# Kernel tuning notes

Hardware: AMD Instinct MI355X
Metric: run time of the kernel (lower is better)

Reference implementation:

```python
import jax, jax.numpy as jnp
import numpy as np
from jax import lax

EPS = 1e-5
DN = ('NCHW', 'OIHW', 'NCHW')

def _sign(v):
    # (v >= 0) * 2 - 1
    return jnp.where(v >= 0, 1.0, -1.0).astype(v.dtype)

def _conv(x, w, b):
    y = lax.conv_general_dilated(x, w, (1, 1), 'VALID', dimension_numbers=DN)
    return y + b[None, :, None, None]

def _bn(x):
    # BatchNorm2d(affine=False), training mode: biased batch stats over (N,H,W)
    m = jnp.mean(x, axis=(0, 2, 3), keepdims=True)
    v = jnp.var(x, axis=(0, 2, 3), keepdims=True)
    return (x - m) * lax.rsqrt(v + EPS)

def setup_inputs() -> dict:
    key = jax.random.key(0)
    ks = jax.random.split(key, 9)
    f = jnp.float32
    B = 8192
    x = jax.random.normal(ks[0], (B, 1, 28, 28), dtype=f)
    # conv params, clipped to [-1, 1] as in clip_weights()
    w1 = jnp.clip(jax.random.normal(ks[1], (32, 1, 9, 9), dtype=f) * 0.1, -1, 1)
    b1 = jnp.clip(jax.random.normal(ks[2], (32,), dtype=f) * 0.1, -1, 1)
    w2 = jnp.clip(jax.random.normal(ks[3], (16, 32, 9, 9), dtype=f) * 0.1, -1, 1)
    b2 = jnp.clip(jax.random.normal(ks[4], (16,), dtype=f) * 0.1, -1, 1)
    w3 = jnp.clip(jax.random.normal(ks[5], (8, 16, 9, 9), dtype=f) * 0.1, -1, 1)
    b3 = jnp.clip(jax.random.normal(ks[6], (8,), dtype=f) * 0.1, -1, 1)
    wl = jnp.clip(jax.random.normal(ks[7], (10, 8, 4, 4), dtype=f) * 0.1, -1, 1)
    bl = jnp.clip(jax.random.normal(ks[8], (10,), dtype=f) * 0.1, -1, 1)
    return {"x": x, "w1": w1, "b1": b1, "w2": w2, "b2": b2,
            "w3": w3, "b3": b3, "wl": wl, "bl": bl}

def _block(x, w, b, act=True, norm=True, binarized=True):
    if binarized:
        w, b = _sign(w), _sign(b)
    x = _conv(x, w, b)
    if norm:
        x = _bn(x)
    if act:
        x = _sign(x) if binarized else jax.nn.relu(x)
    return x

def reference(x, w1, b1, w2, b2, w3, b3, wl, bl):
    x = _sign(x)                        # binarize input activations
    x = _block(x, w1, b1)               # (B, 32, 20, 20)
    x = _block(x, w2, b2)               # (B, 16, 12, 12)
    x = _block(x, w3, b3)               # (B,  8,  4,  4)
    x = _block(x, wl, bl, act=False, norm=False)  # (B, 10, 1, 1), binarized weights
    return x.reshape(-1, 10)
```

## Files before the change

### kernel.cpp

```cpp
#include <hip/hip_runtime.h>
#include <stdint.h>

#define BATCH 8192

#define OFF_W1R3    0
#define OFF_W2T     1152
#define OFF_W3B     6336
#define OFF_WLB     8928
#define OFF_SBL     9088
#define OFF_TTOT    9216
#define OFF_T2      9600
#define OFF_S3      9664
#define OFF_S2PART  9728
#define OFF_Z2      534528
#define OFF_Z3      38283264

__global__ __launch_bounds__(256) void k0_pack(const float* __restrict__ w1,
                                               const float* __restrict__ w2,
                                               const float* __restrict__ w3,
                                               const float* __restrict__ wl,
                                               const float* __restrict__ bl,
                                               uint8_t* __restrict__ ws) {
  uint32_t* W1R3 = (uint32_t*)(ws + OFF_W1R3);
  uint32_t* W2T  = (uint32_t*)(ws + OFF_W2T);
  uint32_t* W3B  = (uint32_t*)(ws + OFF_W3B);
  uint64_t* WLB  = (uint64_t*)(ws + OFF_WLB);
  float*    SBL  = (float*)(ws + OFF_SBL);
  int tid = threadIdx.x;
  for (int e = tid; e < 96; e += 256) {
    int oc = e / 3, i = e % 3;
    uint32_t m = 0;
    for (int rr = 0; rr < 3; ++rr)
      for (int kw = 0; kw < 9; ++kw)
        if (w1[oc*81 + (3*i+rr)*9 + kw] < 0.f) m |= 1u << (rr*9 + kw);
    W1R3[e] = m;
  }
  for (int e = tid; e < 1296; e += 256) {
    int k = e >> 4, oc = e & 15;
    uint32_t m = 0;
    for (int ic = 0; ic < 32; ++ic)
      if (w2[(oc*32 + ic)*81 + k] < 0.f) m |= 1u << ic;
    W2T[e] = m;
  }
  for (int e = tid; e < 648; e += 256) {
    int oc = e / 81, k = e % 81;
    uint32_t m = 0;
    for (int ic = 0; ic < 16; ++ic)
      if (w3[(oc*16 + ic)*81 + k] < 0.f) m |= 1u << ic;
    W3B[e] = m;
  }
  for (int e = tid; e < 20; e += 256) {
    int oc = e >> 1, word = e & 1;
    uint64_t m = 0;
    for (int b = 0; b < 64; ++b)
      if (wl[oc*128 + word*64 + b] < 0.f) m |= 1ull << b;
    WLB[e] = m;
  }
  if (tid < 10) SBL[tid] = (bl[tid] >= 0.f) ? 1.f : -1.f;
}

__global__ __launch_bounds__(256) void k1_tsum(const float* __restrict__ x,
                                               uint8_t* __restrict__ ws) {
  int* Ttot = (int*)(ws + OFF_TTOT);
  __shared__ uint16_t RP[4][28][29];
  __shared__ uint16_t P[4][29][29];
  __shared__ int Tacc[81];
  const int tid = threadIdx.x;
  const int wv = tid >> 6, ln = tid & 63;
  if (tid < 81) Tacc[tid] = 0;
  __syncthreads();
  for (int it = 0; it < 2; ++it) {
    int img = blockIdx.x * 8 + it * 4 + wv;
    const float* xi = x + (size_t)img * 784;
    if (ln < 28) {
      uint16_t cnt = 0;
      RP[wv][ln][0] = 0;
      for (int c = 0; c < 28; ++c) {
        cnt += (xi[ln*28 + c] < 0.f) ? 1 : 0;
        RP[wv][ln][c+1] = cnt;
      }
    }
    __syncthreads();
    if (ln < 29) {
      uint16_t run = 0;
      P[wv][0][ln] = 0;
      for (int i = 1; i <= 28; ++i) {
        run += RP[wv][i-1][ln];
        P[wv][i][ln] = run;
      }
    }
    __syncthreads();
    if (ln < 81) {
      int kh = ln / 9, kw = ln % 9;
      int cnt = (int)P[wv][kh+20][kw+20] - (int)P[wv][kh][kw+20]
              - (int)P[wv][kh+20][kw]  + (int)P[wv][kh][kw];
      atomicAdd(&Tacc[ln], 400 - 2*cnt);
    }
    __syncthreads();
  }
  if (tid < 81) atomicAdd(&Ttot[tid], Tacc[tid]);
}

#define K2_IMGS 8
__global__ __launch_bounds__(256) void k2_conv12(const float* __restrict__ x,
                                                 uint8_t* __restrict__ ws) {
  const uint32_t* W1R3g = (const uint32_t*)(ws + OFF_W1R3);
  const uint32_t* W2Tg  = (const uint32_t*)(ws + OFF_W2T);
  const int* Ttot = (const int*)(ws + OFF_TTOT);
  int* S2P = (int*)(ws + OFF_S2PART);

  __shared__ uint32_t __attribute__((aligned(16))) rowm[K2_IMGS*28];
  __shared__ uint32_t __attribute__((aligned(16))) w1r3[96];
  __shared__ uint32_t __attribute__((aligned(16))) w2t[1296];
  __shared__ int tlds[81];
  __shared__ int t1s[32];
  __shared__ uint32_t __attribute__((aligned(16))) A1s[K2_IMGS*400];
  __shared__ int s2acc[16];

  const int tid = threadIdx.x;
  const int img0 = blockIdx.x * K2_IMGS;

  for (int e = tid; e < 96; e += 256)   w1r3[e] = W1R3g[e];
  for (int e = tid; e < 1296; e += 256) w2t[e]  = W2Tg[e];
  if (tid < 81) tlds[tid] = Ttot[tid];
  if (tid < 16) s2acc[tid] = 0;
  if (tid < K2_IMGS*28) {
    int il = tid / 28, rr = tid % 28;
    const float4* xr = (const float4*)(x + (size_t)(img0 + il) * 784 + rr * 28);
    uint32_t m = 0;
    #pragma unroll
    for (int j = 0; j < 7; ++j) {
      float4 v = xr[j];
      if (v.x < 0.f) m |= 1u << (j*4+0);
      if (v.y < 0.f) m |= 1u << (j*4+1);
      if (v.z < 0.f) m |= 1u << (j*4+2);
      if (v.w < 0.f) m |= 1u << (j*4+3);
    }
    rowm[tid] = m;
  }
  __syncthreads();

  if (tid < 32) {
    long long S = 0;
    for (int kh = 0; kh < 9; ++kh)
      for (int kw = 0; kw < 9; ++kw) {
        int bit = (w1r3[tid*3 + kh/3] >> ((kh%3)*9 + kw)) & 1;
        S += (long long)(1 - 2*bit) * tlds[kh*9 + kw];
      }
    const long long N1 = (long long)BATCH * 400;
    long long q = S / N1, rr = S % N1;
    long long t = q + (rr > 0 ? 1 : 0);
    if ((t & 1) == 0) t += 1;
    t1s[tid] = (int)t;
  }
  __syncthreads();

  for (int G = tid; G < K2_IMGS*80; G += 256) {
    int il = G / 80, rem = G - il*80;
    int oh = rem >> 2, ow0 = (rem & 3) * 5;
    uint32_t R[9];
    #pragma unroll
    for (int i = 0; i < 9; ++i) R[i] = rowm[il*28 + oh + i];
    uint32_t win[5][3];
    #pragma unroll
    for (int j = 0; j < 5; ++j) {
      int ow = ow0 + j;
      #pragma unroll
      for (int i = 0; i < 3; ++i) {
        uint32_t b0 = (R[3*i]   >> ow) & 0x1FFu;
        uint32_t b1 = (R[3*i+1] >> ow) & 0x1FFu;
        uint32_t b2 = (R[3*i+2] >> ow) & 0x1FFu;
        win[j][i] = b0 | (b1 << 9) | (b2 << 18);
      }
    }
    uint32_t mask[5] = {0,0,0,0,0};
    #pragma unroll
    for (int ocg = 0; ocg < 4; ++ocg) {
      const uint4* wp = (const uint4*)&w1r3[ocg*24];
      uint32_t wr[24];
      #pragma unroll
      for (int q = 0; q < 6; ++q) {
        uint4 v = wp[q];
        wr[q*4+0]=v.x; wr[q*4+1]=v.y; wr[q*4+2]=v.z; wr[q*4+3]=v.w;
      }
      #pragma unroll
      for (int o8 = 0; o8 < 8; ++o8) {
        int oc = ocg*8 + o8;
        int t = t1s[oc];
        #pragma unroll
        for (int j = 0; j < 5; ++j) {
          int mm = __popc(win[j][0] ^ wr[o8*3])
                 + __popc(win[j][1] ^ wr[o8*3+1])
                 + __popc(win[j][2] ^ wr[o8*3+2]);
          mask[j] |= (uint32_t)((81 - 2*mm) < t) << oc;
        }
      }
    }
    #pragma unroll
    for (int j = 0; j < 5; ++j) A1s[il*400 + oh*20 + ow0 + j] = mask[j];
  }
  __syncthreads();

  uint32_t* Z2w = (uint32_t*)(ws + OFF_Z2);
  const int och = tid & 7, oc0 = och << 1;
  int sl0 = 0, sl1 = 0;
  for (int r = 0; r < 3; ++r) {
    int G = tid + r*256;
    int il = G / 96, rem = G - il*96;
    int oy = rem >> 3;
    const uint32_t* A = &A1s[il*400 + oy*20];
    int acc0[12], acc1[12];
    #pragma unroll
    for (int p = 0; p < 12; ++p) { acc0[p] = 0; acc1[p] = 0; }
    for (int kh = 0; kh < 9; ++kh) {
      const uint4* ar = (const uint4*)(A + kh*20);
      uint32_t a[20];
      #pragma unroll
      for (int q = 0; q < 5; ++q) {
        uint4 v = ar[q];
        a[q*4+0]=v.x; a[q*4+1]=v.y; a[q*4+2]=v.z; a[q*4+3]=v.w;
      }
      uint32_t wv0[9], wv1[9];
      #pragma unroll
      for (int kw = 0; kw < 9; ++kw) {
        uint2 wv = *(const uint2*)&w2t[(kh*9 + kw)*16 + oc0];
        wv0[kw] = wv.x; wv1[kw] = wv.y;
      }
      #pragma unroll
      for (int kw = 0; kw < 9; ++kw) {
        #pragma unroll
        for (int px = 0; px < 12; ++px) {
          acc0[px] += __popc(a[kw+px] ^ wv0[kw]);
          acc1[px] += __popc(a[kw+px] ^ wv1[kw]);
        }
      }
    }
    size_t base0 = (size_t)(img0+il)*1152 + (size_t)oc0*72 + oy*6;
    uint32_t u0[6], u1[6];
    #pragma unroll
    for (int h2 = 0; h2 < 6; ++h2) {
      int za = 2592 - 2*acc0[2*h2], zb = 2592 - 2*acc0[2*h2+1];
      sl0 += za + zb;
      u0[h2] = (uint32_t)(uint16_t)(int16_t)za | ((uint32_t)(uint16_t)(int16_t)zb << 16);
      int zc = 2592 - 2*acc1[2*h2], zd = 2592 - 2*acc1[2*h2+1];
      sl1 += zc + zd;
      u1[h2] = (uint32_t)(uint16_t)(int16_t)zc | ((uint32_t)(uint16_t)(int16_t)zd << 16);
    }
    uint2* p0 = (uint2*)(Z2w + base0);
    p0[0] = make_uint2(u0[0], u0[1]); p0[1] = make_uint2(u0[2], u0[3]); p0[2] = make_uint2(u0[4], u0[5]);
    uint2* p1 = (uint2*)(Z2w + base0 + 72);
    p1[0] = make_uint2(u1[0], u1[1]); p1[1] = make_uint2(u1[2], u1[3]); p1[2] = make_uint2(u1[4], u1[5]);
  }
  atomicAdd(&s2acc[oc0],   sl0);
  atomicAdd(&s2acc[oc0+1], sl1);
  __syncthreads();
  if (tid < 16) S2P[blockIdx.x*16 + tid] = s2acc[tid];
}

__global__ __launch_bounds__(256) void k2b_reduce(uint8_t* __restrict__ ws) {
  const int* S2P = (const int*)(ws + OFF_S2PART);
  int* T2 = (int*)(ws + OFF_T2);
  __shared__ long long part[256];
  int tid = threadIdx.x;
  int c = tid & 15, g = tid >> 4;
  long long s = 0;
  for (int b = g*64; b < g*64 + 64; ++b) s += S2P[b*16 + c];
  part[tid] = s;
  __syncthreads();
  if (tid < 16) {
    long long S = 0;
    for (int g2 = 0; g2 < 16; ++g2) S += part[g2*16 + tid];
    const long long N2 = (long long)BATCH * 144;
    long long q = S / N2, r = S % N2;
    long long t = q + (r > 0 ? 1 : 0);
    if (t & 1) t += 1;
    T2[tid] = (int)t;
  }
}

__global__ __launch_bounds__(256) void k3_conv3(uint8_t* __restrict__ ws) {
  const int16_t* Z2 = (const int16_t*)(ws + OFF_Z2);
  const int* T2 = (const int*)(ws + OFF_T2);
  const uint32_t* W3Bg = (const uint32_t*)(ws + OFF_W3B);
  int16_t* Z3 = (int16_t*)(ws + OFF_Z3);
  unsigned long long* S3 = (unsigned long long*)(ws + OFF_S3);

  __shared__ uint32_t w3b[648];
  __shared__ int t2[16];
  __shared__ uint32_t A2[2][144];
  __shared__ int s3acc[8];

  const int tid = threadIdx.x;
  for (int e = tid; e < 648; e += 256) w3b[e] = W3Bg[e];
  if (tid < 16) t2[tid] = T2[tid];
  if (tid < 8) s3acc[tid] = 0;
  __syncthreads();

  const int half = tid >> 7, h = tid & 127;
  for (int it = 0; it < 4; ++it) {
    int img = blockIdx.x * 8 + it*2 + half;
    const int16_t* z2i = Z2 + (size_t)img * 2304;
    for (int p = h; p < 144; p += 128) {
      uint32_t m = 0;
      #pragma unroll
      for (int ic = 0; ic < 16; ++ic)
        if ((int)z2i[ic*144 + p] < t2[ic]) m |= 1u << ic;
      A2[half][p] = m;
    }
    __syncthreads();
    {
      int oc = h >> 4, pix = h & 15;
      int oy = pix >> 2, ox = pix & 3;
      int mism = 0;
      for (int kh = 0; kh < 9; ++kh)
        #pragma unroll
        for (int kw = 0; kw < 9; ++kw)
          mism += __popc(A2[half][(oy+kh)*12 + ox + kw] ^ w3b[oc*81 + kh*9 + kw]);
      int z3 = 1296 - 2*mism;
      Z3[(size_t)img*128 + h] = (int16_t)z3;
      atomicAdd(&s3acc[oc], z3);
    }
    __syncthreads();
  }
  if (tid < 8)
    atomicAdd(&S3[tid], (unsigned long long)(long long)s3acc[tid]);
}

__global__ __launch_bounds__(256) void k4_final(uint8_t* __restrict__ ws,
                                               float* __restrict__ out) {
  const int16_t* Z3 = (const int16_t*)(ws + OFF_Z3);
  const long long* S3 = (const long long*)(ws + OFF_S3);
  const uint64_t* WLBg = (const uint64_t*)(ws + OFF_WLB);
  const float* SBLg = (const float*)(ws + OFF_SBL);
  __shared__ int t3[8];
  __shared__ uint64_t wlb[20];
  __shared__ float sbl[10];
  const int tid = threadIdx.x;
  if (tid < 8) {
    long long S = S3[tid];
    const long long N3 = (long long)BATCH * 16;
    long long q = S / N3, r = S % N3;
    long long t = q + (r > 0 ? 1 : 0);
    if (t & 1) t += 1;
    t3[tid] = (int)t;
  }
  if (tid < 20) wlb[tid] = WLBg[tid];
  if (tid < 10) sbl[tid] = SBLg[tid];
  __syncthreads();
  int img = blockIdx.x * 256 + tid;
  const int16_t* z3i = Z3 + (size_t)img * 128;
  uint64_t a0 = 0, a1 = 0;
  for (int j = 0; j < 64; ++j)
    if ((int)z3i[j] < t3[j >> 4]) a0 |= 1ull << j;
  for (int j = 0; j < 64; ++j)
    if ((int)z3i[64 + j] < t3[(64 + j) >> 4]) a1 |= 1ull << j;
  #pragma unroll
  for (int oc = 0; oc < 10; ++oc) {
    int mism = __popcll(a0 ^ wlb[oc*2]) + __popcll(a1 ^ wlb[oc*2 + 1]);
    out[(size_t)img*10 + oc] = (float)(128 - 2*mism) + sbl[oc];
  }
}

extern "C" void kernel_launch(void* const* d_in, const int* in_sizes, int n_in,
                              void* d_out, int out_size, void* d_ws, size_t ws_size,
                              hipStream_t stream) {
  (void)in_sizes; (void)n_in; (void)out_size; (void)ws_size;
  const float* x  = (const float*)d_in[0];
  const float* w1 = (const float*)d_in[1];
  const float* w2 = (const float*)d_in[3];
  const float* w3 = (const float*)d_in[5];
  const float* wl = (const float*)d_in[7];
  const float* bl = (const float*)d_in[8];
  uint8_t* ws = (uint8_t*)d_ws;
  float* out = (float*)d_out;

  hipMemsetAsync(ws + OFF_TTOT, 0, 512, stream);
  k0_pack<<<1, 256, 0, stream>>>(w1, w2, w3, wl, bl, ws);
  k1_tsum<<<1024, 256, 0, stream>>>(x, ws);
  k2_conv12<<<1024, 256, 0, stream>>>(x, ws);
  k2b_reduce<<<1, 256, 0, stream>>>(ws);
  k3_conv3<<<1024, 256, 0, stream>>>(ws);
  k4_final<<<32, 256, 0, stream>>>(ws, out);
}
```

Before: 301.5 us.

## Fuse pack/reduce kernels, use bitmask popcount tsum, repack Z2/Z3 layouts

Folds weight packing into the input-statistics kernel and recomputes the input window sums from row bitmasks with popcount and a sliding window, instead of 2D prefix sums in shared memory. The separate BN2 reduction kernel is merged into conv3, which now handles 32 images per block. Z2 is switched to a pixel-major interleaved layout so conv3 can build its bitmasks from vectorized loads, and Z3 is read with uint4 loads. These changes cut kernel launches and strided global reads, but every conv3 block now redundantly re-reduces the S2 partial sums, and the padded weight layouts must match their indexing exactly.

After: 257.8 us. 1.17x faster.

```diff
diff --git a/kernel.cpp b/kernel.cpp
--- a/kernel.cpp
+++ b/kernel.cpp
@@ -3,101 +3,125 @@
 
 #define BATCH 8192
 
-#define OFF_W1R3    0
-#define OFF_W2T     1152
-#define OFF_W3B     6336
-#define OFF_WLB     8928
-#define OFF_SBL     9088
-#define OFF_TTOT    9216
-#define OFF_T2      9600
-#define OFF_S3      9664
-#define OFF_S2PART  9728
-#define OFF_Z2      534528
-#define OFF_Z3      38283264
-
-__global__ __launch_bounds__(256) void k0_pack(const float* __restrict__ w1,
-                                               const float* __restrict__ w2,
-                                               const float* __restrict__ w3,
-                                               const float* __restrict__ wl,
-                                               const float* __restrict__ bl,
-                                               uint8_t* __restrict__ ws) {
-  uint32_t* W1R3 = (uint32_t*)(ws + OFF_W1R3);
-  uint32_t* W2T  = (uint32_t*)(ws + OFF_W2T);
-  uint32_t* W3B  = (uint32_t*)(ws + OFF_W3B);
-  uint64_t* WLB  = (uint64_t*)(ws + OFF_WLB);
-  float*    SBL  = (float*)(ws + OFF_SBL);
-  int tid = threadIdx.x;
-  for (int e = tid; e < 96; e += 256) {
-    int oc = e / 3, i = e % 3;
-    uint32_t m = 0;
-    for (int rr = 0; rr < 3; ++rr)
-      for (int kw = 0; kw < 9; ++kw)
-        if (w1[oc*81 + (3*i+rr)*9 + kw] < 0.f) m |= 1u << (rr*9 + kw);
-    W1R3[e] = m;
-  }
-  for (int e = tid; e < 1296; e += 256) {
-    int k = e >> 4, oc = e & 15;
-    uint32_t m = 0;
-    for (int ic = 0; ic < 32; ++ic)
-      if (w2[(oc*32 + ic)*81 + k] < 0.f) m |= 1u << ic;
-    W2T[e] = m;
-  }
-  for (int e = tid; e < 648; e += 256) {
-    int oc = e / 81, k = e % 81;
-    uint32_t m = 0;
-    for (int ic = 0; ic < 16; ++ic)
-      if (w3[(oc*16 + ic)*81 + k] < 0.f) m |= 1u << ic;
-    W3B[e] = m;
-  }
-  for (int e = tid; e < 20; e += 256) {
-    int oc = e >> 1, word = e & 1;
-    uint64_t m = 0;
-    for (int b = 0; b < 64; ++b)
-      if (wl[oc*128 + word*64 + b] < 0.f) m |= 1ull << b;
-    WLB[e] = m;
-  }
-  if (tid < 10) SBL[tid] = (bl[tid] >= 0.f) ? 1.f : -1.f;
-}
-
-__global__ __launch_bounds__(256) void k1_tsum(const float* __restrict__ x,
-                                               uint8_t* __restrict__ ws) {
+#define OFF_W1R3   0
+#define OFF_W2P    384
+#define OFF_W3P    6144
+#define OFF_WLB    9600
+#define OFF_SBL    9760
+#define OFF_TTOT   9856
+#define OFF_S3     10184
+#define OFF_S2PART 10496
+#define OFF_Z2     76800
+#define OFF_Z3     37825792
+
+__global__ __launch_bounds__(256) void k1_pack_tsum(const float* __restrict__ x,
+                                                    const float* __restrict__ w1,
+                                                    const float* __restrict__ w2,
+                                                    const float* __restrict__ w3,
+                                                    const float* __restrict__ wl,
+                                                    const float* __restrict__ bl,
+                                                    uint8_t* __restrict__ ws) {
   int* Ttot = (int*)(ws + OFF_TTOT);
-  __shared__ uint16_t RP[4][28][29];
-  __shared__ uint16_t P[4][29][29];
+  const int tid = threadIdx.x;
+
+  if (blockIdx.x == 0) {
+    uint32_t* W1R3 = (uint32_t*)(ws + OFF_W1R3);
+    uint32_t* W2P  = (uint32_t*)(ws + OFF_W2P);
+    uint32_t* W3P  = (uint32_t*)(ws + OFF_W3P);
+    uint64_t* WLB  = (uint64_t*)(ws + OFF_WLB);
+    float*    SBL  = (float*)(ws + OFF_SBL);
+    for (int e = tid; e < 96; e += 256) {
+      int oc = e / 3, i = e % 3;
+      uint32_t m = 0;
+      for (int rr = 0; rr < 3; ++rr)
+        for (int kw = 0; kw < 9; ++kw)
+          if (w1[oc*81 + (3*i+rr)*9 + kw] < 0.f) m |= 1u << (rr*9 + kw);
+      W1R3[e] = m;
+    }
+    for (int e = tid; e < 648; e += 256) {
+      int och = e / 81, k = e % 81;
+      int kh = k / 9, kw = k % 9;
+      uint32_t m0 = 0, m1 = 0;
+      int oc0 = och*2;
+      for (int ic = 0; ic < 32; ++ic) {
+        if (w2[(oc0*32 + ic)*81 + k] < 0.f)     m0 |= 1u << ic;
+        if (w2[((oc0+1)*32 + ic)*81 + k] < 0.f) m1 |= 1u << ic;
+      }
+      int idx = ((och*9 + kh)*10 + kw)*2;
+      W2P[idx] = m0; W2P[idx+1] = m1;
+    }
+    for (int e = tid; e < 72; e += 256) {
+      int idx = (e*10 + 9)*2;
+      W2P[idx] = 0; W2P[idx+1] = 0;
+    }
+    for (int e = tid; e < 648; e += 256) {
+      int oc = e / 81, k = e % 81;
+      int kh = k / 9, kw = k % 9;
+      uint32_t m = 0;
+      for (int ic = 0; ic < 16; ++ic)
+        if (w3[(oc*16 + ic)*81 + k] < 0.f) m |= 1u << ic;
+      W3P[(oc*9 + kh)*12 + kw] = m;
+    }
+    for (int e = tid; e < 216; e += 256) {
+      int row = e / 3, p = e % 3;
+      W3P[row*12 + 9 + p] = 0;
+    }
+    for (int e = tid; e < 20; e += 256) {
+      int oc = e >> 1, word = e & 1;
+      uint64_t m = 0;
+      for (int b = 0; b < 64; ++b)
+        if (wl[oc*128 + word*64 + b] < 0.f) m |= 1ull << b;
+      WLB[e] = m;
+    }
+    if (tid < 10) SBL[tid] = (bl[tid] >= 0.f) ? 1.f : -1.f;
+  }
+
+  __shared__ uint32_t rowm[896];
   __shared__ int Tacc[81];
-  const int tid = threadIdx.x;
-  const int wv = tid >> 6, ln = tid & 63;
   if (tid < 81) Tacc[tid] = 0;
   __syncthreads();
-  for (int it = 0; it < 2; ++it) {
-    int img = blockIdx.x * 8 + it * 4 + wv;
-    const float* xi = x + (size_t)img * 784;
-    if (ln < 28) {
-      uint16_t cnt = 0;
-      RP[wv][ln][0] = 0;
-      for (int c = 0; c < 28; ++c) {
-        cnt += (xi[ln*28 + c] < 0.f) ? 1 : 0;
-        RP[wv][ln][c+1] = cnt;
-      }
-    }
-    __syncthreads();
-    if (ln < 29) {
-      uint16_t run = 0;
-      P[wv][0][ln] = 0;
-      for (int i = 1; i <= 28; ++i) {
-        run += RP[wv][i-1][ln];
-        P[wv][i][ln] = run;
-      }
-    }
-    __syncthreads();
-    if (ln < 81) {
-      int kh = ln / 9, kw = ln % 9;
-      int cnt = (int)P[wv][kh+20][kw+20] - (int)P[wv][kh][kw+20]
-              - (int)P[wv][kh+20][kw]  + (int)P[wv][kh][kw];
-      atomicAdd(&Tacc[ln], 400 - 2*cnt);
-    }
-    __syncthreads();
-  }
+
+  const int img0 = blockIdx.x * 32;
+  #pragma unroll
+  for (int it = 0; it < 4; ++it) {
+    int R = tid + it*256;
+    if (R < 896) {
+      int il = R / 28, r = R % 28;
+      const float4* xr = (const float4*)(x + (size_t)(img0 + il) * 784 + r * 28);
+      uint32_t m = 0;
+      #pragma unroll
+      for (int j = 0; j < 7; ++j) {
+        float4 v = xr[j];
+        if (v.x < 0.f) m |= 1u << (j*4+0);
+        if (v.y < 0.f) m |= 1u << (j*4+1);
+        if (v.z < 0.f) m |= 1u << (j*4+2);
+        if (v.w < 0.f) m |= 1u << (j*4+3);
+      }
+      rowm[R] = m;
+    }
+  }
+  __syncthreads();
+
+  for (int T = tid; T < 288; T += 256) {
+    int il = T / 9, kw = T % 9;
+    int base = il * 28;
+    int n9[9];
+    int sum20 = 0;
+    #pragma unroll
+    for (int r = 0; r < 20; ++r) {
+      int n = __popc((rowm[base + r] >> kw) & 0xFFFFFu);
+      if (r < 9) n9[r] = n;
+      sum20 += n;
+    }
+    atomicAdd(&Tacc[kw], 400 - 2*sum20);
+    #pragma unroll
+    for (int kh = 1; kh <= 8; ++kh) {
+      int nadd = __popc((rowm[base + kh + 19] >> kw) & 0xFFFFFu);
+      sum20 += nadd - n9[kh-1];
+      atomicAdd(&Tacc[kh*9 + kw], 400 - 2*sum20);
+    }
+  }
+  __syncthreads();
   if (tid < 81) atomicAdd(&Ttot[tid], Tacc[tid]);
 }
 
@@ -105,13 +129,13 @@
 __global__ __launch_bounds__(256) void k2_conv12(const float* __restrict__ x,
                                                  uint8_t* __restrict__ ws) {
   const uint32_t* W1R3g = (const uint32_t*)(ws + OFF_W1R3);
-  const uint32_t* W2Tg  = (const uint32_t*)(ws + OFF_W2T);
+  const uint32_t* W2Pg  = (const uint32_t*)(ws + OFF_W2P);
   const int* Ttot = (const int*)(ws + OFF_TTOT);
   int* S2P = (int*)(ws + OFF_S2PART);
 
   __shared__ uint32_t __attribute__((aligned(16))) rowm[K2_IMGS*28];
   __shared__ uint32_t __attribute__((aligned(16))) w1r3[96];
-  __shared__ uint32_t __attribute__((aligned(16))) w2t[1296];
+  __shared__ uint32_t __attribute__((aligned(16))) w2p[1440];
   __shared__ int tlds[81];
   __shared__ int t1s[32];
   __shared__ uint32_t __attribute__((aligned(16))) A1s[K2_IMGS*400];
@@ -121,7 +145,7 @@
   const int img0 = blockIdx.x * K2_IMGS;
 
   for (int e = tid; e < 96; e += 256)   w1r3[e] = W1R3g[e];
-  for (int e = tid; e < 1296; e += 256) w2t[e]  = W2Tg[e];
+  for (int e = tid; e < 1440; e += 256) w2p[e]  = W2Pg[e];
   if (tid < 81) tlds[tid] = Ttot[tid];
   if (tid < 16) s2acc[tid] = 0;
   if (tid < K2_IMGS*28) {
@@ -220,36 +244,31 @@
         uint4 v = ar[q];
         a[q*4+0]=v.x; a[q*4+1]=v.y; a[q*4+2]=v.z; a[q*4+3]=v.w;
       }
-      uint32_t wv0[9], wv1[9];
+      const uint4* wp4 = (const uint4*)&w2p[(och*9 + kh)*20];
+      uint32_t wbuf[20];
+      #pragma unroll
+      for (int q = 0; q < 5; ++q) {
+        uint4 v = wp4[q];
+        wbuf[q*4+0]=v.x; wbuf[q*4+1]=v.y; wbuf[q*4+2]=v.z; wbuf[q*4+3]=v.w;
+      }
       #pragma unroll
       for (int kw = 0; kw < 9; ++kw) {
-        uint2 wv = *(const uint2*)&w2t[(kh*9 + kw)*16 + oc0];
-        wv0[kw] = wv.x; wv1[kw] = wv.y;
-      }
-      #pragma unroll
-      for (int kw = 0; kw < 9; ++kw) {
+        uint32_t w0 = wbuf[2*kw], w1v = wbuf[2*kw+1];
         #pragma unroll
         for (int px = 0; px < 12; ++px) {
-          acc0[px] += __popc(a[kw+px] ^ wv0[kw]);
-          acc1[px] += __popc(a[kw+px] ^ wv1[kw]);
+          acc0[px] += __popc(a[kw+px] ^ w0);
+          acc1[px] += __popc(a[kw+px] ^ w1v);
         }
       }
     }
-    size_t base0 = (size_t)(img0+il)*1152 + (size_t)oc0*72 + oy*6;
-    uint32_t u0[6], u1[6];
-    #pragma unroll
-    for (int h2 = 0; h2 < 6; ++h2) {
-      int za = 2592 - 2*acc0[2*h2], zb = 2592 - 2*acc0[2*h2+1];
-      sl0 += za + zb;
-      u0[h2] = (uint32_t)(uint16_t)(int16_t)za | ((uint32_t)(uint16_t)(int16_t)zb << 16);
-      int zc = 2592 - 2*acc1[2*h2], zd = 2592 - 2*acc1[2*h2+1];
-      sl1 += zc + zd;
-      u1[h2] = (uint32_t)(uint16_t)(int16_t)zc | ((uint32_t)(uint16_t)(int16_t)zd << 16);
-    }
-    uint2* p0 = (uint2*)(Z2w + base0);
-    p0[0] = make_uint2(u0[0], u0[1]); p0[1] = make_uint2(u0[2], u0[3]); p0[2] = make_uint2(u0[4], u0[5]);
-    uint2* p1 = (uint2*)(Z2w + base0 + 72);
-    p1[0] = make_uint2(u1[0], u1[1]); p1[1] = make_uint2(u1[2], u1[3]); p1[2] = make_uint2(u1[4], u1[5]);
+    size_t wbase = (size_t)(img0+il)*1152 + (size_t)oy*96 + och;
+    #pragma unroll
+    for (int px = 0; px < 12; ++px) {
+      int z0 = 2592 - 2*acc0[px], z1v = 2592 - 2*acc1[px];
+      sl0 += z0; sl1 += z1v;
+      Z2w[wbase + px*8] = (uint32_t)(uint16_t)(int16_t)z0
+                        | ((uint32_t)(uint16_t)(int16_t)z1v << 16);
+    }
   }
   atomicAdd(&s2acc[oc0],   sl0);
   atomicAdd(&s2acc[oc0+1], sl1);
@@ -257,78 +276,107 @@
   if (tid < 16) S2P[blockIdx.x*16 + tid] = s2acc[tid];
 }
 
-__global__ __launch_bounds__(256) void k2b_reduce(uint8_t* __restrict__ ws) {
+__global__ __launch_bounds__(256) void k3_conv3(uint8_t* __restrict__ ws) {
   const int* S2P = (const int*)(ws + OFF_S2PART);
-  int* T2 = (int*)(ws + OFF_T2);
-  __shared__ long long part[256];
-  int tid = threadIdx.x;
-  int c = tid & 15, g = tid >> 4;
-  long long s = 0;
-  for (int b = g*64; b < g*64 + 64; ++b) s += S2P[b*16 + c];
-  part[tid] = s;
+  const uint32_t* W3Pg = (const uint32_t*)(ws + OFF_W3P);
+  const uint32_t* Z2w = (const uint32_t*)(ws + OFF_Z2);
+  uint32_t* Z3w = (uint32_t*)(ws + OFF_Z3);
+  unsigned long long* S3 = (unsigned long long*)(ws + OFF_S3);
+
+  __shared__ uint32_t __attribute__((aligned(16))) w3p[864];
+  __shared__ int part[256];
+  __shared__ int t2s[16];
+  __shared__ uint32_t __attribute__((aligned(16))) A2[32*144];
+  __shared__ int s3acc[8];
+
+  const int tid = threadIdx.x;
+  const int img0 = blockIdx.x * 32;
+
+  {
+    int c = tid & 15, g = tid >> 4;
+    int s = 0;
+    for (int j = 0; j < 64; ++j) s += S2P[(g + 16*j)*16 + c];
+    part[tid] = s;
+  }
+  for (int e = tid; e < 864; e += 256) w3p[e] = W3Pg[e];
+  if (tid < 8) s3acc[tid] = 0;
   __syncthreads();
   if (tid < 16) {
     long long S = 0;
-    for (int g2 = 0; g2 < 16; ++g2) S += part[g2*16 + tid];
+    #pragma unroll
+    for (int g = 0; g < 16; ++g) S += (long long)part[g*16 + tid];
     const long long N2 = (long long)BATCH * 144;
     long long q = S / N2, r = S % N2;
     long long t = q + (r > 0 ? 1 : 0);
     if (t & 1) t += 1;
-    T2[tid] = (int)t;
-  }
-}
-
-__global__ __launch_bounds__(256) void k3_conv3(uint8_t* __restrict__ ws) {
-  const int16_t* Z2 = (const int16_t*)(ws + OFF_Z2);
-  const int* T2 = (const int*)(ws + OFF_T2);
-  const uint32_t* W3Bg = (const uint32_t*)(ws + OFF_W3B);
-  int16_t* Z3 = (int16_t*)(ws + OFF_Z3);
-  unsigned long long* S3 = (unsigned long long*)(ws + OFF_S3);
-
-  __shared__ uint32_t w3b[648];
-  __shared__ int t2[16];
-  __shared__ uint32_t A2[2][144];
-  __shared__ int s3acc[8];
-
-  const int tid = threadIdx.x;
-  for (int e = tid; e < 648; e += 256) w3b[e] = W3Bg[e];
-  if (tid < 16) t2[tid] = T2[tid];
-  if (tid < 8) s3acc[tid] = 0;
-  __syncthreads();
-
-  const int half = tid >> 7, h = tid & 127;
-  for (int it = 0; it < 4; ++it) {
-    int img = blockIdx.x * 8 + it*2 + half;
-    const int16_t* z2i = Z2 + (size_t)img * 2304;
-    for (int p = h; p < 144; p += 128) {
-      uint32_t m = 0;
-      #pragma unroll
-      for (int ic = 0; ic < 16; ++ic)
-        if ((int)z2i[ic*144 + p] < t2[ic]) m |= 1u << ic;
-      A2[half][p] = m;
-    }
-    __syncthreads();
-    {
-      int oc = h >> 4, pix = h & 15;
-      int oy = pix >> 2, ox = pix & 3;
-      int mism = 0;
-      for (int kh = 0; kh < 9; ++kh)
+    t2s[tid] = (int)t;
+  }
+  __syncthreads();
+
+  #pragma unroll
+  for (int j = 0; j < 18; ++j) {
+    int idx = tid + j*256;
+    const uint4* zp = (const uint4*)&Z2w[(size_t)(img0 + idx/144)*1152 + (size_t)(idx%144)*8];
+    uint4 v0 = zp[0], v1 = zp[1];
+    uint32_t zz[8] = {v0.x,v0.y,v0.z,v0.w, v1.x,v1.y,v1.z,v1.w};
+    uint32_t m = 0;
+    #pragma unroll
+    for (int i = 0; i < 8; ++i) {
+      int zlo = (int)(short)(zz[i] & 0xFFFFu);
+      int zhi = (int)zz[i] >> 16;
+      m |= (uint32_t)(zlo < t2s[2*i])   << (2*i);
+      m |= (uint32_t)(zhi < t2s[2*i+1]) << (2*i+1);
+    }
+    A2[idx] = m;
+  }
+  __syncthreads();
+
+  const int il = tid >> 3, oc = tid & 7;
+  int acc[16];
+  #pragma unroll
+  for (int i = 0; i < 16; ++i) acc[i] = 0;
+  #pragma unroll
+  for (int r = 0; r < 12; ++r) {
+    const uint4* ar = (const uint4*)&A2[il*144 + r*12];
+    uint4 v0 = ar[0], v1 = ar[1], v2 = ar[2];
+    uint32_t a[12] = {v0.x,v0.y,v0.z,v0.w, v1.x,v1.y,v1.z,v1.w, v2.x,v2.y,v2.z,v2.w};
+    #pragma unroll
+    for (int oy = 0; oy < 4; ++oy) {
+      if (r - oy >= 0 && r - oy <= 8) {
+        int kh = r - oy;
+        const uint4* wr = (const uint4*)&w3p[(oc*9 + kh)*12];
+        uint4 w0 = wr[0], w1v = wr[1], w2v = wr[2];
+        uint32_t w[9] = {w0.x,w0.y,w0.z,w0.w, w1v.x,w1v.y,w1v.z,w1v.w, w2v.x};
         #pragma unroll
-        for (int kw = 0; kw < 9; ++kw)
-          mism += __popc(A2[half][(oy+kh)*12 + ox + kw] ^ w3b[oc*81 + kh*9 + kw]);
-      int z3 = 1296 - 2*mism;
-      Z3[(size_t)img*128 + h] = (int16_t)z3;
-      atomicAdd(&s3acc[oc], z3);
-    }
-    __syncthreads();
-  }
+        for (int ox = 0; ox < 4; ++ox) {
+          int m = 0;
+          #pragma unroll
+          for (int kw = 0; kw < 9; ++kw) m += __popc(a[ox+kw] ^ w[kw]);
+          acc[oy*4+ox] += m;
+        }
+      }
+    }
+  }
+  int ssum = 0;
+  uint32_t packed[8];
+  #pragma unroll
+  for (int h = 0; h < 8; ++h) {
+    int za = 1296 - 2*acc[2*h], zb = 1296 - 2*acc[2*h+1];
+    ssum += za + zb;
+    packed[h] = (uint32_t)(uint16_t)(int16_t)za | ((uint32_t)(uint16_t)(int16_t)zb << 16);
+  }
+  uint4* zp = (uint4*)&Z3w[(size_t)(img0 + il)*64 + oc*8];
+  zp[0] = make_uint4(packed[0], packed[1], packed[2], packed[3]);
+  zp[1] = make_uint4(packed[4], packed[5], packed[6], packed[7]);
+  atomicAdd(&s3acc[oc], ssum);
+  __syncthreads();
   if (tid < 8)
     atomicAdd(&S3[tid], (unsigned long long)(long long)s3acc[tid]);
 }
 
 __global__ __launch_bounds__(256) void k4_final(uint8_t* __restrict__ ws,
-                                               float* __restrict__ out) {
-  const int16_t* Z3 = (const int16_t*)(ws + OFF_Z3);
+                                                float* __restrict__ out) {
+  const uint32_t* Z3w = (const uint32_t*)(ws + OFF_Z3);
   const long long* S3 = (const long long*)(ws + OFF_S3);
   const uint64_t* WLBg = (const uint64_t*)(ws + OFF_WLB);
   const float* SBLg = (const float*)(ws + OFF_SBL);
@@ -348,12 +396,24 @@
   if (tid < 10) sbl[tid] = SBLg[tid];
   __syncthreads();
   int img = blockIdx.x * 256 + tid;
-  const int16_t* z3i = Z3 + (size_t)img * 128;
+  const uint4* zp = (const uint4*)&Z3w[(size_t)img * 64];
+  uint32_t zz[64];
+  #pragma unroll
+  for (int q = 0; q < 16; ++q) {
+    uint4 v = zp[q];
+    zz[q*4+0]=v.x; zz[q*4+1]=v.y; zz[q*4+2]=v.z; zz[q*4+3]=v.w;
+  }
   uint64_t a0 = 0, a1 = 0;
-  for (int j = 0; j < 64; ++j)
-    if ((int)z3i[j] < t3[j >> 4]) a0 |= 1ull << j;
-  for (int j = 0; j < 64; ++j)
-    if ((int)z3i[64 + j] < t3[(64 + j) >> 4]) a1 |= 1ull << j;
+  #pragma unroll
+  for (int j = 0; j < 64; ++j) {
+    int z = (j & 1) ? ((int)zz[j>>1] >> 16) : (int)(short)(zz[j>>1] & 0xFFFFu);
+    a0 |= (uint64_t)(z < t3[j >> 4]) << j;
+  }
+  #pragma unroll
+  for (int j = 0; j < 64; ++j) {
+    int z = (j & 1) ? ((int)zz[32 + (j>>1)] >> 16) : (int)(short)(zz[32 + (j>>1)] & 0xFFFFu);
+    a1 |= (uint64_t)(z < t3[(64 + j) >> 4]) << j;
+  }
   #pragma unroll
   for (int oc = 0; oc < 10; ++oc) {
     int mism = __popcll(a0 ^ wlb[oc*2]) + __popcll(a1 ^ wlb[oc*2 + 1]);
@@ -374,11 +434,9 @@
   uint8_t* ws = (uint8_t*)d_ws;
   float* out = (float*)d_out;
 
-  hipMemsetAsync(ws + OFF_TTOT, 0, 512, stream);
-  k0_pack<<<1, 256, 0, stream>>>(w1, w2, w3, wl, bl, ws);
-  k1_tsum<<<1024, 256, 0, stream>>>(x, ws);
+  hipMemsetAsync(ws + OFF_TTOT, 0, 400, stream);
+  k1_pack_tsum<<<256, 256, 0, stream>>>(x, w1, w2, w3, wl, bl, ws);
   k2_conv12<<<1024, 256, 0, stream>>>(x, ws);
-  k2b_reduce<<<1, 256, 0, stream>>>(ws);
-  k3_conv3<<<1024, 256, 0, stream>>>(ws);
+  k3_conv3<<<256, 256, 0, stream>>>(ws);
   k4_final<<<32, 256, 0, stream>>>(ws, out);
 }
```
